# Kernel optimization log

Measured on AMD Instinct MI355X. Metric: run time of the kernel, lower is better.

The kernel has to match this reference:

```python
import jax, jax.numpy as jnp
import numpy as np

DIM = 1024

def setup_inputs() -> dict:
    key = jax.random.key(0)
    k1, k2, k3, k4, k5 = jax.random.split(key, 5)
    x = jax.random.normal(k1, (8, 2048, DIM), dtype=jnp.float32)
    # nn.Linear-style params: W is [out, in], b is [out]
    s = 1.0 / np.sqrt(DIM)
    W1 = jax.random.uniform(k2, (DIM, DIM), jnp.float32, -s, s)
    b1 = jax.random.uniform(k3, (DIM,), jnp.float32, -s, s)
    W2 = jax.random.uniform(k4, (DIM, DIM), jnp.float32, -s, s)
    b2 = jax.random.uniform(k5, (DIM,), jnp.float32, -s, s)
    return {"x": x, "W1": W1, "b1": b1, "W2": W2, "b2": b2}

def reference(x, W1, b1, W2, b2):
    # NOTE: original module reuses linear_1 for BOTH V and Q (linear_3 unused)
    V = x @ W1.T + b1                      # [B,S,D]
    K = x @ W2.T + b2                      # [B,S,D]
    Q = x @ W1.T + b1                      # [B,S,D]
    scale = 1.0 / jnp.sqrt(jnp.float32(x.shape[-1]))
    scores = jnp.einsum('bkd,bqd->bkq', K, Q) * scale  # K @ Q^T, [B,S,S]
    attn = jax.nn.softmax(scores, axis=-1)
    out = jnp.einsum('bkq,bqd->bkd', attn, V)
    return out
```

## Files before the change

### kernel.cpp

```cpp
#include <hip/hip_runtime.h>
#include <hip/hip_fp16.h>
#include <cstdint>
#include <cstddef>

#define DIMK 1024
#define NBATCH 8
#define SEQ 2048

typedef _Float16 half8 __attribute__((ext_vector_type(8)));
typedef _Float16 half4_t __attribute__((ext_vector_type(4)));
typedef float float4_t __attribute__((ext_vector_type(4)));

__device__ __forceinline__ void gload16(const _Float16* g, _Float16* l) {
  __builtin_amdgcn_global_load_lds((const __attribute__((address_space(1))) void*)g,
                                   (__attribute__((address_space(3))) void*)l, 16, 0, 0);
}

#define BAR() __builtin_amdgcn_s_barrier()
#define LGKM0() asm volatile("s_waitcnt lgkmcnt(0)" ::: "memory")
#define VMW(n) asm volatile("s_waitcnt vmcnt(" #n ")" ::: "memory")

template<bool SUMA>
__device__ __forceinline__ void gemm256_core(
    const char* __restrict__ Ab, const char* __restrict__ Bb,
    int ldA, int ldB, int NT, _Float16* lds,
    float4_t (&acc)[8][4], float (&rsum)[8])
{
  const int tid = threadIdx.x;
  const int lane = tid & 63, wave = tid >> 6;
  const int warp_m = wave >> 2, warp_n = wave & 3;
  const int srow = lane >> 3;
  const int scb = ((lane & 7) ^ srow) << 4;
  const int c0 = wave * 2;
  const int fr = lane & 15, fg = lane >> 4, rsw = lane & 7;

  half8 Af[4][2], Bf0[2][2], Bf1[2][2];

#define STG(tau, h) do { \
    const int _h = (h); \
    const bool _isA = (_h == 0) || (_h == 3); \
    const int _rh = (_h >= 2) ? 128 : 0; \
    const char* _gb = _isA ? Ab : Bb; \
    const int _ld = _isA ? ldA : ldB; \
    _Float16* _lb = lds + (((tau) & 1) ? 32768 : 0) + (_isA ? 0 : 16384) + _rh * 64 + c0 * 512; \
    const char* _g0 = _gb + (size_t)(_rh + c0 * 8 + srow) * _ld + (tau) * 128 + scb; \
    gload16((const _Float16*)_g0, _lb); \
    gload16((const _Float16*)(_g0 + (size_t)8 * _ld), _lb + 512); \
  } while (0)

#define LDA2(par, g) do { \
    const _Float16* _ab = lds + ((par) ? 32768 : 0); \
    _Pragma("unroll") for (int m = 0; m < 4; ++m) { \
      const int _row = warp_m * 64 + (g) * 128 + m * 16 + fr; \
      _Pragma("unroll") for (int kk = 0; kk < 2; ++kk) \
        Af[m][kk] = *(const half8*)(_ab + _row * 64 + (((kk * 4 + fg) ^ rsw) << 3)); \
    } } while (0)

#define LDB2(par, g, BF) do { \
    const _Float16* _bb = lds + ((par) ? 32768 : 0) + 16384; \
    _Pragma("unroll") for (int n = 0; n < 2; ++n) { \
      const int _row = warp_n * 32 + (g) * 128 + n * 16 + fr; \
      _Pragma("unroll") for (int kk = 0; kk < 2; ++kk) \
        BF[n][kk] = *(const half8*)(_bb + _row * 64 + (((kk * 4 + fg) ^ rsw) << 3)); \
    } } while (0)

#define QUAD(gm, gn, BF) do { \
    _Pragma("unroll") for (int m = 0; m < 4; ++m) \
    _Pragma("unroll") for (int n = 0; n < 2; ++n) \
    _Pragma("unroll") for (int kk = 0; kk < 2; ++kk) \
      acc[(gm) * 4 + m][(gn) * 2 + n] = __builtin_amdgcn_mfma_f32_16x16x32_f16( \
          Af[m][kk], BF[n][kk], acc[(gm) * 4 + m][(gn) * 2 + n], 0, 0, 0); \
  } while (0)

#define ASUM(g) do { if constexpr (SUMA) { \
    _Pragma("unroll") for (int m = 0; m < 4; ++m) { float _s = 0.f; \
      _Pragma("unroll") for (int kk = 0; kk < 2; ++kk) \
      _Pragma("unroll") for (int j = 0; j < 8; ++j) _s += (float)Af[m][kk][j]; \
      rsum[(g) * 4 + m] += _s; } } } while (0)

  STG(0, 0); STG(0, 1); STG(0, 2); STG(0, 3);
  STG(1, 0); STG(1, 1); STG(1, 2);
  VMW(6);
  BAR();

  int t = 0;
  for (; t + 2 < NT; ++t) {
    const int par = t & 1;
    LDA2(par, 0); LDB2(par, 0, Bf0);
    STG(t + 1, 3);
    BAR(); LGKM0();
    __builtin_amdgcn_s_setprio(1); QUAD(0, 0, Bf0); __builtin_amdgcn_s_setprio(0);
    ASUM(0);
    BAR();
    LDB2(par, 1, Bf1);
    STG(t + 2, 0);
    BAR(); LGKM0();
    __builtin_amdgcn_s_setprio(1); QUAD(0, 1, Bf1); __builtin_amdgcn_s_setprio(0);
    BAR();
    LDA2(par, 1);
    STG(t + 2, 1);
    BAR(); LGKM0();
    __builtin_amdgcn_s_setprio(1); QUAD(1, 1, Bf1); __builtin_amdgcn_s_setprio(0);
    ASUM(1);
    BAR();
    STG(t + 2, 2);
    BAR();
    __builtin_amdgcn_s_setprio(1); QUAD(1, 0, Bf0); __builtin_amdgcn_s_setprio(0);
    VMW(6);
    BAR();
  }
  {
    const int par = t & 1;
    LDA2(par, 0); LDB2(par, 0, Bf0);
    STG(NT - 1, 3);
    BAR(); LGKM0();
    __builtin_amdgcn_s_setprio(1); QUAD(0, 0, Bf0); __builtin_amdgcn_s_setprio(0);
    ASUM(0);
    BAR();
    LDB2(par, 1, Bf1);
    BAR(); LGKM0();
    __builtin_amdgcn_s_setprio(1); QUAD(0, 1, Bf1); __builtin_amdgcn_s_setprio(0);
    BAR();
    LDA2(par, 1);
    BAR(); LGKM0();
    __builtin_amdgcn_s_setprio(1); QUAD(1, 1, Bf1); __builtin_amdgcn_s_setprio(0);
    ASUM(1);
    BAR();
    __builtin_amdgcn_s_setprio(1); QUAD(1, 0, Bf0); __builtin_amdgcn_s_setprio(0);
    VMW(0);
    BAR();
  }
  {
    const int par = (NT - 1) & 1;
    LDA2(par, 0); LDB2(par, 0, Bf0); LDB2(par, 1, Bf1);
    QUAD(0, 0, Bf0); QUAD(0, 1, Bf1);
    ASUM(0);
    LDA2(par, 1);
    QUAD(1, 1, Bf1); QUAD(1, 0, Bf0);
    ASUM(1);
  }
#undef STG
#undef LDA2
#undef LDB2
#undef QUAD
#undef ASUM
}

#define ROW_LOCAL(mi) (warp_m * 64 + ((mi) & 3) * 16 + (((mi) >> 2) ? 128 : 0))
#define COL_LOCAL(nj) (warp_n * 32 + (((nj) & 1) ? 16 : 0) + (((nj) >> 1) ? 128 : 0))

__global__ __launch_bounds__(256) void prep_kernel(const float* __restrict__ x,
                                                   const float* __restrict__ W1,
                                                   const float* __restrict__ W2,
                                                   _Float16* __restrict__ xh,
                                                   _Float16* __restrict__ Wcat) {
  int i = blockIdx.x * 256 + threadIdx.x;
  if (i < 4194304) {
    float4_t v = ((const float4_t*)x)[i];
    half4_t h; h[0]=(_Float16)v[0]; h[1]=(_Float16)v[1]; h[2]=(_Float16)v[2]; h[3]=(_Float16)v[3];
    ((half4_t*)xh)[i] = h;
  } else if (i < 4456448) {
    int j = i - 4194304;
    float4_t v = ((const float4_t*)W1)[j];
    half4_t h; h[0]=(_Float16)v[0]; h[1]=(_Float16)v[1]; h[2]=(_Float16)v[2]; h[3]=(_Float16)v[3];
    ((half4_t*)Wcat)[j] = h;
  } else if (i < 4718592) {
    int j = i - 4456448;
    float4_t v = ((const float4_t*)W2)[j];
    half4_t h; h[0]=(_Float16)v[0]; h[1]=(_Float16)v[1]; h[2]=(_Float16)v[2]; h[3]=(_Float16)v[3];
    ((half4_t*)(Wcat + 1048576))[j] = h;
  }
}

__global__ __launch_bounds__(512, 2) void gemm_vk_kernel(
    const _Float16* __restrict__ xh, const _Float16* __restrict__ Wcat,
    const float* __restrict__ b1, const float* __restrict__ b2,
    _Float16* __restrict__ Vbuf, _Float16* __restrict__ Kbuf,
    _Float16* __restrict__ Vt) {
  __shared__ _Float16 lds[65536];
  const int tid = threadIdx.x, lane = tid & 63, wave = tid >> 6;
  const int warp_m = wave >> 2, warp_n = wave & 3;
  const int fr = lane & 15, rb = (lane >> 4) * 4;
  const int flat = blockIdx.x;
  const int wg = (flat & 7) * 64 + (flat >> 3);
  const int bm = wg >> 3, bn = wg & 7;
  const bool isV = bn < 4;
  const float* bias = isV ? b1 : b2;
  const int ncol0 = (bn & 3) * 256;
  float bv[4];
#pragma unroll
  for (int nj = 0; nj < 4; ++nj) bv[nj] = bias[ncol0 + COL_LOCAL(nj) + fr];

  float4_t acc[8][4] = {};
  float rsum[8];
  gemm256_core<false>((const char*)(xh + (size_t)bm * 256 * DIMK),
                      (const char*)(Wcat + (size_t)bn * 256 * DIMK),
                      DIMK * 2, DIMK * 2, DIMK / 64, lds, acc, rsum);

  _Float16* dst = isV ? Vbuf : Kbuf;
#pragma unroll
  for (int mi = 0; mi < 8; ++mi) {
    const int row = bm * 256 + ROW_LOCAL(mi) + rb;
#pragma unroll
    for (int nj = 0; nj < 4; ++nj) {
      const int col = ncol0 + COL_LOCAL(nj) + fr;
#pragma unroll
      for (int r = 0; r < 4; ++r)
        dst[(size_t)(row + r) * DIMK + col] = (_Float16)(acc[mi][nj][r] + bv[nj]);
    }
  }
  if (isV) {
    __syncthreads();
#pragma unroll
    for (int mi = 0; mi < 8; ++mi) {
      const int q0 = ROW_LOCAL(mi) + rb;
#pragma unroll
      for (int nj = 0; nj < 4; ++nj) {
        const int d = COL_LOCAL(nj) + fr;
        const float bb = bv[nj];
#pragma unroll
        for (int r = 0; r < 4; ++r) {
          const int q = q0 + r;
          lds[d * 256 + ((((q >> 3) ^ d) & 31) << 3) + (q & 7)] = (_Float16)(acc[mi][nj][r] + bb);
        }
      }
    }
    __syncthreads();
    const int b = bm >> 3, qb = (bm & 7) * 256;
    const size_t vtb = ((size_t)b * DIMK + ncol0) * SEQ + qb;
#pragma unroll
    for (int i = 0; i < 16; ++i) {
      const int idx = tid + i * 512;
      const int d = idx >> 5, G = idx & 31;
      half8 v = *(const half8*)(lds + d * 256 + (((G ^ d) & 31) << 3));
      *(half8*)(Vt + vtb + (size_t)d * SEQ + G * 8) = v;
    }
  }
}

__global__ __launch_bounds__(512, 2) void gemm_scores_kernel(
    const _Float16* __restrict__ Kb, const _Float16* __restrict__ Vb,
    _Float16* __restrict__ P) {
  __shared__ _Float16 lds[65536];
  const int tid = threadIdx.x, lane = tid & 63, wave = tid >> 6;
  const int warp_m = wave >> 2, warp_n = wave & 3;
  const int fr = lane & 15, rb = (lane >> 4) * 4;
  const int flat = blockIdx.x;
  const int wg = (flat & 7) * 64 + (flat >> 3);
  const int b = wg >> 6, loc = wg & 63, bm = loc >> 3, bn = loc & 7;

  float4_t acc[8][4] = {};
  float rsum[8];
  gemm256_core<false>((const char*)(Kb + (size_t)(b * SEQ + bm * 256) * DIMK),
                      (const char*)(Vb + (size_t)(b * SEQ + bn * 256) * DIMK),
                      DIMK * 2, DIMK * 2, DIMK / 64, lds, acc, rsum);

  _Float16* Pb = P + (size_t)b * SEQ * SEQ;
#pragma unroll
  for (int mi = 0; mi < 8; ++mi) {
    const int row = bm * 256 + ROW_LOCAL(mi) + rb;
#pragma unroll
    for (int nj = 0; nj < 4; ++nj) {
      const int col = bn * 256 + COL_LOCAL(nj) + fr;
#pragma unroll
      for (int r = 0; r < 4; ++r)
        Pb[(size_t)(row + r) * SEQ + col] = (_Float16)__expf(acc[mi][nj][r] * 0.03125f);
    }
  }
}

__global__ __launch_bounds__(512, 2) void gemm_out_kernel(
    const _Float16* __restrict__ P, const _Float16* __restrict__ Vt,
    float* __restrict__ out) {
  __shared__ _Float16 lds[65536];
  const int tid = threadIdx.x, lane = tid & 63, wave = tid >> 6;
  const int warp_m = wave >> 2, warp_n = wave & 3;
  const int fr = lane & 15, rb = (lane >> 4) * 4;
  const int flat = blockIdx.x;
  const int wg = (flat & 7) * 32 + (flat >> 3);
  const int b = wg >> 5, loc = wg & 31, bm = loc >> 2, bn = loc & 3;

  float4_t acc[8][4] = {};
  float rsum[8] = {0.f, 0.f, 0.f, 0.f, 0.f, 0.f, 0.f, 0.f};
  gemm256_core<true>((const char*)(P + (size_t)(b * SEQ + bm * 256) * SEQ),
                     (const char*)(Vt + (size_t)(b * DIMK + bn * 256) * SEQ),
                     SEQ * 2, SEQ * 2, SEQ / 64, lds, acc, rsum);

  float* ob = out + ((size_t)b * SEQ + bm * 256) * DIMK + bn * 256;
#pragma unroll
  for (int mi = 0; mi < 8; ++mi) {
    float s = rsum[mi];
    s += __shfl_xor(s, 16, 64);
    s += __shfl_xor(s, 32, 64);
#pragma unroll
    for (int r = 0; r < 4; ++r) {
      const float inv = __builtin_amdgcn_rcpf(__shfl(s, rb + r, 64));
      const int row = ROW_LOCAL(mi) + rb + r;
#pragma unroll
      for (int nj = 0; nj < 4; ++nj) {
        const int col = COL_LOCAL(nj) + fr;
        ob[(size_t)row * DIMK + col] = acc[mi][nj][r] * inv;
      }
    }
  }
}

extern "C" void kernel_launch(void* const* d_in, const int* in_sizes, int n_in,
                              void* d_out, int out_size, void* d_ws, size_t ws_size,
                              hipStream_t stream) {
  const float* x  = (const float*)d_in[0];
  const float* W1 = (const float*)d_in[1];
  const float* b1 = (const float*)d_in[2];
  const float* W2 = (const float*)d_in[3];
  const float* b2 = (const float*)d_in[4];
  float* out = (float*)d_out;

  char* ws = (char*)d_ws;
  _Float16* xh   = (_Float16*)(ws);
  _Float16* Pbuf = (_Float16*)(ws);
  _Float16* Vt   = (_Float16*)(ws + 67108864);
  _Float16* Vbuf = (_Float16*)(ws + 100663296);
  _Float16* Kbuf = (_Float16*)(ws + 134217728);
  _Float16* Wcat = (_Float16*)(ws + 167772160);

  prep_kernel<<<18432, 256, 0, stream>>>(x, W1, W2, xh, Wcat);
  gemm_vk_kernel<<<512, 512, 0, stream>>>(xh, Wcat, b1, b2, Vbuf, Kbuf, Vt);
  gemm_scores_kernel<<<512, 512, 0, stream>>>(Kbuf, Vbuf, Pbuf);
  gemm_out_kernel<<<256, 512, 0, stream>>>(Pbuf, Vt, out);
}
```

Measured before the change: 345.0 us.

## Compute softmax row sums in scores epilogue and precompute LDS/global addresses

```diff
diff --git a/kernel.cpp b/kernel.cpp
--- a/kernel.cpp
+++ b/kernel.cpp
@@ -19,12 +19,13 @@
 #define BAR() __builtin_amdgcn_s_barrier()
 #define LGKM0() asm volatile("s_waitcnt lgkmcnt(0)" ::: "memory")
 #define VMW(n) asm volatile("s_waitcnt vmcnt(" #n ")" ::: "memory")
-
-template<bool SUMA>
+#define PRIO1() __builtin_amdgcn_s_setprio(1)
+#define PRIO0() __builtin_amdgcn_s_setprio(0)
+
 __device__ __forceinline__ void gemm256_core(
     const char* __restrict__ Ab, const char* __restrict__ Bb,
-    int ldA, int ldB, int NT, _Float16* lds,
-    float4_t (&acc)[8][4], float (&rsum)[8])
+    const int ldA, const int ldB, const int NT, _Float16* lds,
+    float4_t (&acc)[8][4])
 {
   const int tid = threadIdx.x;
   const int lane = tid & 63, wave = tid >> 6;
@@ -34,34 +35,40 @@
   const int c0 = wave * 2;
   const int fr = lane & 15, fg = lane >> 4, rsw = lane & 7;
 
+  const int xo0 = (fg ^ rsw) << 3;
+  const int xo1 = ((4 + fg) ^ rsw) << 3;
+  const int aro = (warp_m * 64 + fr) * 64;
+  const int bro = 16384 + (warp_n * 32 + fr) * 64;
+
+  _Float16* const sA = lds + c0 * 512;
+  _Float16* const sB = lds + 16384 + c0 * 512;
+  const char* const gA = Ab + (size_t)(c0 * 8 + srow) * ldA + scb;
+  const char* const gB = Bb + (size_t)(c0 * 8 + srow) * ldB + scb;
+  const size_t ldA8 = (size_t)ldA * 8,   ldB8 = (size_t)ldB * 8;
+  const size_t ldA128 = (size_t)ldA * 128, ldB128 = (size_t)ldB * 128;
+
   half8 Af[4][2], Bf0[2][2], Bf1[2][2];
 
-#define STG(tau, h) do { \
-    const int _h = (h); \
-    const bool _isA = (_h == 0) || (_h == 3); \
-    const int _rh = (_h >= 2) ? 128 : 0; \
-    const char* _gb = _isA ? Ab : Bb; \
-    const int _ld = _isA ? ldA : ldB; \
-    _Float16* _lb = lds + (((tau) & 1) ? 32768 : 0) + (_isA ? 0 : 16384) + _rh * 64 + c0 * 512; \
-    const char* _g0 = _gb + (size_t)(_rh + c0 * 8 + srow) * _ld + (tau) * 128 + scb; \
-    gload16((const _Float16*)_g0, _lb); \
-    gload16((const _Float16*)(_g0 + (size_t)8 * _ld), _lb + 512); \
-  } while (0)
-
-#define LDA2(par, g) do { \
-    const _Float16* _ab = lds + ((par) ? 32768 : 0); \
+#define STG_A(pbuf, ob_, bot) do { \
+    _Float16* _lb = sA + (pbuf) + ((bot) ? 8192 : 0); \
+    const char* _g = gA + ((bot) ? ldA128 : 0) + (size_t)(ob_); \
+    gload16((const _Float16*)_g, _lb); \
+    gload16((const _Float16*)(_g + ldA8), _lb + 512); } while (0)
+#define STG_B(pbuf, ob_, bot) do { \
+    _Float16* _lb = sB + (pbuf) + ((bot) ? 8192 : 0); \
+    const char* _g = gB + ((bot) ? ldB128 : 0) + (size_t)(ob_); \
+    gload16((const _Float16*)_g, _lb); \
+    gload16((const _Float16*)(_g + ldB8), _lb + 512); } while (0)
+
+#define LDA2(g) do { \
     _Pragma("unroll") for (int m = 0; m < 4; ++m) { \
-      const int _row = warp_m * 64 + (g) * 128 + m * 16 + fr; \
-      _Pragma("unroll") for (int kk = 0; kk < 2; ++kk) \
-        Af[m][kk] = *(const half8*)(_ab + _row * 64 + (((kk * 4 + fg) ^ rsw) << 3)); \
+      Af[m][0] = *(const half8*)(pA0 + (g) * 8192 + m * 1024); \
+      Af[m][1] = *(const half8*)(pA1 + (g) * 8192 + m * 1024); \
     } } while (0)
-
-#define LDB2(par, g, BF) do { \
-    const _Float16* _bb = lds + ((par) ? 32768 : 0) + 16384; \
+#define LDB2(g, BF) do { \
     _Pragma("unroll") for (int n = 0; n < 2; ++n) { \
-      const int _row = warp_n * 32 + (g) * 128 + n * 16 + fr; \
-      _Pragma("unroll") for (int kk = 0; kk < 2; ++kk) \
-        BF[n][kk] = *(const half8*)(_bb + _row * 64 + (((kk * 4 + fg) ^ rsw) << 3)); \
+      BF[n][0] = *(const half8*)(pB0 + (g) * 8192 + n * 1024); \
+      BF[n][1] = *(const half8*)(pB1 + (g) * 8192 + n * 1024); \
     } } while (0)
 
 #define QUAD(gm, gn, BF) do { \
@@ -72,78 +79,82 @@
           Af[m][kk], BF[n][kk], acc[(gm) * 4 + m][(gn) * 2 + n], 0, 0, 0); \
   } while (0)
 
-#define ASUM(g) do { if constexpr (SUMA) { \
-    _Pragma("unroll") for (int m = 0; m < 4; ++m) { float _s = 0.f; \
-      _Pragma("unroll") for (int kk = 0; kk < 2; ++kk) \
-      _Pragma("unroll") for (int j = 0; j < 8; ++j) _s += (float)Af[m][kk][j]; \
-      rsum[(g) * 4 + m] += _s; } } } while (0)
-
-  STG(0, 0); STG(0, 1); STG(0, 2); STG(0, 3);
-  STG(1, 0); STG(1, 1); STG(1, 2);
+  STG_A(0, 0, 0); STG_B(0, 0, 0); STG_B(0, 0, 1); STG_A(0, 0, 1);
+  STG_A(32768, 128, 0); STG_B(32768, 128, 0); STG_B(32768, 128, 1);
   VMW(6);
   BAR();
 
   int t = 0;
   for (; t + 2 < NT; ++t) {
-    const int par = t & 1;
-    LDA2(par, 0); LDB2(par, 0, Bf0);
-    STG(t + 1, 3);
-    BAR(); LGKM0();
-    __builtin_amdgcn_s_setprio(1); QUAD(0, 0, Bf0); __builtin_amdgcn_s_setprio(0);
-    ASUM(0);
-    BAR();
-    LDB2(par, 1, Bf1);
-    STG(t + 2, 0);
-    BAR(); LGKM0();
-    __builtin_amdgcn_s_setprio(1); QUAD(0, 1, Bf1); __builtin_amdgcn_s_setprio(0);
-    BAR();
-    LDA2(par, 1);
-    STG(t + 2, 1);
-    BAR(); LGKM0();
-    __builtin_amdgcn_s_setprio(1); QUAD(1, 1, Bf1); __builtin_amdgcn_s_setprio(0);
-    ASUM(1);
-    BAR();
-    STG(t + 2, 2);
-    BAR();
-    __builtin_amdgcn_s_setprio(1); QUAD(1, 0, Bf0); __builtin_amdgcn_s_setprio(0);
+    const int pb  = (t & 1) << 15;
+    const int pbn = pb ^ 32768;
+    const int o1 = (t + 1) << 7, o2 = (t + 2) << 7;
+    const _Float16* pA0 = lds + pb + aro + xo0;
+    const _Float16* pA1 = lds + pb + aro + xo1;
+    const _Float16* pB0 = lds + pb + bro + xo0;
+    const _Float16* pB1 = lds + pb + bro + xo1;
+    LDA2(0); LDB2(0, Bf0);
+    STG_A(pbn, o1, 1);
+    BAR(); LGKM0();
+    PRIO1(); QUAD(0, 0, Bf0); PRIO0();
+    BAR();
+    LDB2(1, Bf1);
+    STG_A(pb, o2, 0);
+    BAR(); LGKM0();
+    PRIO1(); QUAD(0, 1, Bf1); PRIO0();
+    BAR();
+    LDA2(1);
+    STG_B(pb, o2, 0);
+    BAR(); LGKM0();
+    PRIO1(); QUAD(1, 1, Bf1); PRIO0();
+    BAR();
+    STG_B(pb, o2, 1);
+    BAR();
+    PRIO1(); QUAD(1, 0, Bf0); PRIO0();
     VMW(6);
     BAR();
   }
   {
-    const int par = t & 1;
-    LDA2(par, 0); LDB2(par, 0, Bf0);
-    STG(NT - 1, 3);
-    BAR(); LGKM0();
-    __builtin_amdgcn_s_setprio(1); QUAD(0, 0, Bf0); __builtin_amdgcn_s_setprio(0);
-    ASUM(0);
-    BAR();
-    LDB2(par, 1, Bf1);
-    BAR(); LGKM0();
-    __builtin_amdgcn_s_setprio(1); QUAD(0, 1, Bf1); __builtin_amdgcn_s_setprio(0);
-    BAR();
-    LDA2(par, 1);
-    BAR(); LGKM0();
-    __builtin_amdgcn_s_setprio(1); QUAD(1, 1, Bf1); __builtin_amdgcn_s_setprio(0);
-    ASUM(1);
-    BAR();
-    __builtin_amdgcn_s_setprio(1); QUAD(1, 0, Bf0); __builtin_amdgcn_s_setprio(0);
+    const int pb  = (t & 1) << 15;
+    const int pbn = pb ^ 32768;
+    const int oL = (NT - 1) << 7;
+    const _Float16* pA0 = lds + pb + aro + xo0;
+    const _Float16* pA1 = lds + pb + aro + xo1;
+    const _Float16* pB0 = lds + pb + bro + xo0;
+    const _Float16* pB1 = lds + pb + bro + xo1;
+    LDA2(0); LDB2(0, Bf0);
+    STG_A(pbn, oL, 1);
+    BAR(); LGKM0();
+    PRIO1(); QUAD(0, 0, Bf0); PRIO0();
+    BAR();
+    LDB2(1, Bf1);
+    BAR(); LGKM0();
+    PRIO1(); QUAD(0, 1, Bf1); PRIO0();
+    BAR();
+    LDA2(1);
+    BAR(); LGKM0();
+    PRIO1(); QUAD(1, 1, Bf1); PRIO0();
+    BAR();
+    PRIO1(); QUAD(1, 0, Bf0); PRIO0();
     VMW(0);
     BAR();
   }
   {
-    const int par = (NT - 1) & 1;
-    LDA2(par, 0); LDB2(par, 0, Bf0); LDB2(par, 1, Bf1);
+    const int pb = ((NT - 1) & 1) << 15;
+    const _Float16* pA0 = lds + pb + aro + xo0;
+    const _Float16* pA1 = lds + pb + aro + xo1;
+    const _Float16* pB0 = lds + pb + bro + xo0;
+    const _Float16* pB1 = lds + pb + bro + xo1;
+    LDA2(0); LDB2(0, Bf0); LDB2(1, Bf1);
     QUAD(0, 0, Bf0); QUAD(0, 1, Bf1);
-    ASUM(0);
-    LDA2(par, 1);
+    LDA2(1);
     QUAD(1, 1, Bf1); QUAD(1, 0, Bf0);
-    ASUM(1);
-  }
-#undef STG
+  }
+#undef STG_A
+#undef STG_B
 #undef LDA2
 #undef LDB2
 #undef QUAD
-#undef ASUM
 }
 
 #define ROW_LOCAL(mi) (warp_m * 64 + ((mi) & 3) * 16 + (((mi) >> 2) ? 128 : 0))
@@ -192,10 +203,9 @@
   for (int nj = 0; nj < 4; ++nj) bv[nj] = bias[ncol0 + COL_LOCAL(nj) + fr];
 
   float4_t acc[8][4] = {};
-  float rsum[8];
-  gemm256_core<false>((const char*)(xh + (size_t)bm * 256 * DIMK),
-                      (const char*)(Wcat + (size_t)bn * 256 * DIMK),
-                      DIMK * 2, DIMK * 2, DIMK / 64, lds, acc, rsum);
+  gemm256_core((const char*)(xh + (size_t)bm * 256 * DIMK),
+               (const char*)(Wcat + (size_t)bn * 256 * DIMK),
+               DIMK * 2, DIMK * 2, DIMK / 64, lds, acc);
 
   _Float16* dst = isV ? Vbuf : Kbuf;
 #pragma unroll
@@ -240,7 +250,7 @@
 
 __global__ __launch_bounds__(512, 2) void gemm_scores_kernel(
     const _Float16* __restrict__ Kb, const _Float16* __restrict__ Vb,
-    _Float16* __restrict__ P) {
+    _Float16* __restrict__ P, float* __restrict__ rsum_part) {
   __shared__ _Float16 lds[65536];
   const int tid = threadIdx.x, lane = tid & 63, wave = tid >> 6;
   const int warp_m = wave >> 2, warp_n = wave & 3;
@@ -250,28 +260,43 @@
   const int b = wg >> 6, loc = wg & 63, bm = loc >> 3, bn = loc & 7;
 
   float4_t acc[8][4] = {};
-  float rsum[8];
-  gemm256_core<false>((const char*)(Kb + (size_t)(b * SEQ + bm * 256) * DIMK),
-                      (const char*)(Vb + (size_t)(b * SEQ + bn * 256) * DIMK),
-                      DIMK * 2, DIMK * 2, DIMK / 64, lds, acc, rsum);
-
+  gemm256_core((const char*)(Kb + (size_t)(b * SEQ + bm * 256) * DIMK),
+               (const char*)(Vb + (size_t)(b * SEQ + bn * 256) * DIMK),
+               DIMK * 2, DIMK * 2, DIMK / 64, lds, acc);
+
+  __syncthreads();
+  float* part = (float*)lds;
   _Float16* Pb = P + (size_t)b * SEQ * SEQ;
 #pragma unroll
   for (int mi = 0; mi < 8; ++mi) {
-    const int row = bm * 256 + ROW_LOCAL(mi) + rb;
-#pragma unroll
-    for (int nj = 0; nj < 4; ++nj) {
-      const int col = bn * 256 + COL_LOCAL(nj) + fr;
-#pragma unroll
-      for (int r = 0; r < 4; ++r)
-        Pb[(size_t)(row + r) * SEQ + col] = (_Float16)__expf(acc[mi][nj][r] * 0.03125f);
-    }
+    const int rl = ROW_LOCAL(mi) + rb;
+#pragma unroll
+    for (int r = 0; r < 4; ++r) {
+      float s = 0.f;
+#pragma unroll
+      for (int nj = 0; nj < 4; ++nj) {
+        const int col = bn * 256 + COL_LOCAL(nj) + fr;
+        const _Float16 ph = (_Float16)__expf(acc[mi][nj][r] * 0.03125f);
+        Pb[(size_t)(bm * 256 + rl + r) * SEQ + col] = ph;
+        s += (float)ph;
+      }
+      s += __shfl_xor(s, 1, 64);
+      s += __shfl_xor(s, 2, 64);
+      s += __shfl_xor(s, 4, 64);
+      s += __shfl_xor(s, 8, 64);
+      if (fr == 0) part[warp_n * 256 + rl + r] = s;
+    }
+  }
+  __syncthreads();
+  if (tid < 256) {
+    const float s = part[tid] + part[256 + tid] + part[512 + tid] + part[768 + tid];
+    rsum_part[((size_t)b * 8 + bn) * SEQ + bm * 256 + tid] = s;
   }
 }
 
 __global__ __launch_bounds__(512, 2) void gemm_out_kernel(
     const _Float16* __restrict__ P, const _Float16* __restrict__ Vt,
-    float* __restrict__ out) {
+    const float* __restrict__ rsum_part, float* __restrict__ out) {
   __shared__ _Float16 lds[65536];
   const int tid = threadIdx.x, lane = tid & 63, wave = tid >> 6;
   const int warp_m = wave >> 2, warp_n = wave & 3;
@@ -281,21 +306,28 @@
   const int b = wg >> 5, loc = wg & 31, bm = loc >> 2, bn = loc & 3;
 
   float4_t acc[8][4] = {};
-  float rsum[8] = {0.f, 0.f, 0.f, 0.f, 0.f, 0.f, 0.f, 0.f};
-  gemm256_core<true>((const char*)(P + (size_t)(b * SEQ + bm * 256) * SEQ),
-                     (const char*)(Vt + (size_t)(b * DIMK + bn * 256) * SEQ),
-                     SEQ * 2, SEQ * 2, SEQ / 64, lds, acc, rsum);
+  gemm256_core((const char*)(P + (size_t)(b * SEQ + bm * 256) * SEQ),
+               (const char*)(Vt + (size_t)(b * DIMK + bn * 256) * SEQ),
+               SEQ * 2, SEQ * 2, SEQ / 64, lds, acc);
+
+  __syncthreads();
+  float* invf = (float*)lds;
+  if (tid < 256) {
+    const float* rp = rsum_part + (size_t)b * 8 * SEQ + bm * 256 + tid;
+    float s = 0.f;
+#pragma unroll
+    for (int j = 0; j < 8; ++j) s += rp[j * SEQ];
+    invf[tid] = __builtin_amdgcn_rcpf(s);
+  }
+  __syncthreads();
 
   float* ob = out + ((size_t)b * SEQ + bm * 256) * DIMK + bn * 256;
 #pragma unroll
   for (int mi = 0; mi < 8; ++mi) {
-    float s = rsum[mi];
-    s += __shfl_xor(s, 16, 64);
-    s += __shfl_xor(s, 32, 64);
 #pragma unroll
     for (int r = 0; r < 4; ++r) {
-      const float inv = __builtin_amdgcn_rcpf(__shfl(s, rb + r, 64));
       const int row = ROW_LOCAL(mi) + rb + r;
+      const float inv = invf[row];
 #pragma unroll
       for (int nj = 0; nj < 4; ++nj) {
         const int col = COL_LOCAL(nj) + fr;
@@ -322,9 +354,10 @@
   _Float16* Vbuf = (_Float16*)(ws + 100663296);
   _Float16* Kbuf = (_Float16*)(ws + 134217728);
   _Float16* Wcat = (_Float16*)(ws + 167772160);
+  float* rsum_part = (float*)(ws + 167772160);
 
   prep_kernel<<<18432, 256, 0, stream>>>(x, W1, W2, xh, Wcat);
   gemm_vk_kernel<<<512, 512, 0, stream>>>(xh, Wcat, b1, b2, Vbuf, Kbuf, Vt);
-  gemm_scores_kernel<<<512, 512, 0, stream>>>(Kbuf, Vbuf, Pbuf);
-  gemm_out_kernel<<<256, 512, 0, stream>>>(Pbuf, Vt, out);
-}
+  gemm_scores_kernel<<<512, 512, 0, stream>>>(Kbuf, Vbuf, Pbuf, rsum_part);
+  gemm_out_kernel<<<256, 512, 0, stream>>>(Pbuf, Vt, rsum_part, out);
+}
```

Measured after the change: 330.3 us. 4.3% less time.
